# Kernel tuning notes

Hardware: AMD Instinct MI355X
Metric: run time of the kernel (lower is better)

## Reference

```python
import jax, jax.numpy as jnp
import numpy as np

GRID = 8
Q = GRID * GRID


def _resize(x, hw):
    # F.interpolate(mode='bilinear', align_corners=False) == jax.image.resize bilinear (half-pixel)
    return jax.image.resize(x, (x.shape[0], x.shape[1], hw[0], hw[1]), method='bilinear')


def _transform(l1, l2, l3):
    hw = l1.shape[2:]
    return jnp.concatenate([l1, _resize(l2, hw), _resize(l3, hw)], axis=1)


def _mlp(x, w1, b1, w2, b2):
    return jax.nn.relu(x @ w1 + b1) @ w2 + b2


def setup_inputs():
    key = jax.random.key(0)
    ks = jax.random.split(key, 16)
    B = 4
    inp = {}
    shapes = {
        't0_l0': (B, 64, 128, 128), 't0_l1': (B, 256, 128, 128),
        't0_l2': (B, 256, 64, 64), 't0_l3': (B, 256, 32, 32),
        't1_l0': (B, 64, 128, 128), 't1_l1': (B, 256, 128, 128),
        't1_l2': (B, 256, 64, 64), 't1_l3': (B, 256, 32, 32),
    }
    for i, (n, s) in enumerate(shapes.items()):
        inp[n] = jax.random.normal(ks[i], s, dtype=jnp.float32)
    # init_query_bbox: (grid + 0.5) / grid_size, exactly as _init_layers
    xx, yy = jnp.meshgrid(jnp.arange(GRID), jnp.arange(GRID), indexing='ij')
    inp['query_bbox'] = (jnp.stack([xx, yy], -1).reshape(Q, 2).astype(jnp.float32) + 0.5) / GRID
    D = 256
    inp['off_w1'] = jax.random.normal(ks[8], (D, D // 2), dtype=jnp.float32) * 0.05
    inp['off_b1'] = jnp.zeros((D // 2,), jnp.float32)
    inp['off_w2'] = jax.random.normal(ks[9], (D // 2, 2), dtype=jnp.float32) * 0.05
    inp['off_b2'] = jnp.zeros((2,), jnp.float32)
    inp['sc_w1'] = jax.random.normal(ks[10], (D, D // 2), dtype=jnp.float32) * 0.05
    inp['sc_b1'] = jnp.zeros((D // 2,), jnp.float32)
    inp['sc_w2'] = jax.random.normal(ks[11], (D // 2, 1), dtype=jnp.float32) * 0.05
    inp['sc_b2'] = jnp.zeros((1,), jnp.float32)
    return inp


def reference(t0_l0, t0_l1, t0_l2, t0_l3, t1_l0, t1_l1, t1_l2, t1_l3,
              query_bbox, off_w1, off_b1, off_w2, off_b2, sc_w1, sc_b1, sc_w2, sc_b2):
    features = _transform(t0_l1, t0_l2, t0_l3)        # [B, 3C, H, W]
    features_next = _transform(t1_l1, t1_l2, t1_l3)
    B, C, H, W = features.shape
    shape = W
    w = W // GRID // 2                                 # half patch width (=8)
    qb = jnp.broadcast_to(query_bbox[None], (B, Q, 2))
    cp = (qb * shape).astype(jnp.int32)                # [B,Q,2] integer centers

    # ---- make_query_feat: batched patch gather (source uses batch-0 centers for all samples)
    mean_feat = features.mean(axis=1)                  # [B,H,W]
    cp0 = cp[0]                                        # [Q,2]
    rows = cp0[:, 0, None] - w + jnp.arange(2 * w)     # [Q,2w]
    cols = cp0[:, 1, None] - w + jnp.arange(2 * w)     # [Q,2w]
    patches = mean_feat[:, rows[:, :, None], cols[:, None, :]]  # [B,Q,2w,2w]
    D = 4 * w * w
    # source does torch.cat(list_over_q, dim=0).reshape(B, Q, -1): this interleaves
    # query/batch axes; replicate faithfully via transpose-then-reshape
    query_feat = jnp.transpose(patches.reshape(B, Q, D), (1, 0, 2)).reshape(B, Q, D)

    offset = _mlp(query_feat, off_w1, off_b1, off_w2, off_b2)   # [B,Q,2]
    scale = _mlp(query_feat, sc_w1, sc_b1, sc_w2, sc_b2)        # [B,Q,1]
    qb_new = (cp.astype(offset.dtype) + offset * w) / shape

    cps = (qb_new * shape).astype(jnp.int32)           # trunc toward zero == torch .to(int32)
    rs, cs = cps[..., 0] - w, cps[..., 1] - w          # [B,Q]
    re_, ce_ = cps[..., 0] + w, cps[..., 1] + w
    r = jnp.arange(H)
    c = jnp.arange(W)
    # torch slicing: negative start wraps to an empty slice -> require start >= 0;
    # end beyond H/W is clipped automatically by r < re_
    row_m = (r[None, None, :] >= rs[..., None]) & (r[None, None, :] < re_[..., None]) & (rs[..., None] >= 0)
    col_m = (c[None, None, :] >= cs[..., None]) & (c[None, None, :] < ce_[..., None]) & (cs[..., None] >= 0)
    cov = row_m[:, :, :, None] & col_m[:, :, None, :]  # [B,Q,H,W]
    tag = jnp.where(cov, jnp.arange(1, Q + 1)[None, :, None, None], 0)
    last = tag.max(axis=1)                             # [B,H,W]; 0 => pixel untouched
    sw = scale[..., 0]                                 # [B,Q]
    sm = jnp.take_along_axis(sw, jnp.maximum(last - 1, 0).reshape(B, -1), axis=1).reshape(B, H, W)
    scale_map = jnp.where(last > 0, sm, jnp.ones((), sw.dtype))
    return features * scale_map[:, None] + features_next
```

## Files before the change

### kernel.cpp

```cpp
#include <hip/hip_runtime.h>

#define HW1 16384
#define HW2 4096
#define HW3 1024
#define NB  4
#define NCH 256

typedef float f4 __attribute__((ext_vector_type(4)));

__device__ inline float psum8(const float* __restrict__ P, int stride, int idx) {
    float s = 0.f;
    #pragma unroll
    for (int g = 0; g < 8; ++g) s += P[(size_t)g * stride + idx];
    return s;
}

__device__ inline float bilp(const float* __restrict__ P, int stride, int n,
                             int y, int x, float scl, float off) {
    float fy = y * scl - off, fx = x * scl - off;
    float fy0 = floorf(fy), fx0 = floorf(fx);
    float wy = fy - fy0, wx = fx - fx0;
    int y0 = max((int)fy0, 0), y1 = min((int)fy0 + 1, n - 1);
    int x0 = max((int)fx0, 0), x1 = min((int)fx0 + 1, n - 1);
    float m00 = psum8(P, stride, y0 * n + x0), m01 = psum8(P, stride, y0 * n + x1);
    float m10 = psum8(P, stride, y1 * n + x0), m11 = psum8(P, stride, y1 * n + x1);
    float a = m00 * (1.f - wx) + m01 * wx;
    float b = m10 * (1.f - wx) + m11 * wx;
    return a * (1.f - wy) + b * wy;
}

__global__ __launch_bounds__(256) void k_sumsA(
    const float* __restrict__ l1, const float* __restrict__ l2, const float* __restrict__ l3,
    float* __restrict__ P1, float* __restrict__ P2, float* __restrict__ P3) {
    int t = threadIdx.x, blk = blockIdx.x;
    const float* src; float* dst; int hw, px0, b, cg;
    if (blk < 512) {
        b = blk >> 7; cg = (blk >> 4) & 7; int q = blk & 15;
        hw = HW1; src = l1; dst = P1; px0 = q * 1024;
    } else if (blk < 640) {
        int k = blk - 512; b = k >> 5; cg = (k >> 2) & 7; int q = k & 3;
        hw = HW2; src = l2; dst = P2; px0 = q * 1024;
    } else {
        int k = blk - 640; b = k >> 3; cg = k & 7;
        hw = HW3; src = l3; dst = P3; px0 = 0;
    }
    const f4* s = (const f4*)(src + ((size_t)(b * NCH + cg * 32)) * hw + px0);
    int hw4 = hw >> 2;
    f4 acc = {0.f, 0.f, 0.f, 0.f};
    #pragma unroll 8
    for (int c = 0; c < 32; ++c)
        acc += s[(size_t)c * hw4 + t];
    ((f4*)(dst + ((size_t)(b * 8 + cg)) * hw + px0))[t] = acc;
}

__global__ __launch_bounds__(256) void k_query(
    const float* __restrict__ P1, const float* __restrict__ P2, const float* __restrict__ P3,
    const float* __restrict__ qb,
    const float* __restrict__ ow1, const float* __restrict__ ob1,
    const float* __restrict__ ow2, const float* __restrict__ ob2,
    const float* __restrict__ sw1, const float* __restrict__ sb1,
    const float* __restrict__ sw2, const float* __restrict__ sb2,
    int* __restrict__ RS, int* __restrict__ CS, float* __restrict__ SC) {
    __shared__ float feat[256];
    __shared__ float hid[256];
    __shared__ float res[3];
    int n = blockIdx.x, t = threadIdx.x;
    int b = n & 3, qp = n >> 2;
    int qi = qp >> 3, qj = qp & 7;
    {
        int i = t >> 4, j = t & 15;
        int y = 16 * qi + i, x = 16 * qj + j;
        const float* P1b = P1 + (size_t)b * 8 * HW1;
        const float* P2b = P2 + (size_t)b * 8 * HW2;
        const float* P3b = P3 + (size_t)b * 8 * HW3;
        float v = psum8(P1b, HW1, y * 128 + x);
        v += bilp(P2b, HW2, 64, y, x, 0.5f, 0.25f);
        v += bilp(P3b, HW3, 32, y, x, 0.25f, 0.375f);
        feat[t] = v * (1.0f / 768.0f);
    }
    __syncthreads();
    {
        int h = t & 127;
        const float* W  = (t < 128) ? ow1 : sw1;
        const float* Bv = (t < 128) ? ob1 : sb1;
        float acc = 0.f;
        #pragma unroll 8
        for (int d = 0; d < 256; ++d)
            acc = fmaf(feat[d], W[d * 128 + h], acc);
        hid[t] = fmaxf(acc + Bv[h], 0.f);
    }
    __syncthreads();
    int w = t >> 6, l = t & 63;
    if (w < 3) {
        float acc;
        if (w == 0)      acc = fmaf(hid[l], ow2[2 * l],     hid[l + 64] * ow2[2 * l + 128]);
        else if (w == 1) acc = fmaf(hid[l], ow2[2 * l + 1], hid[l + 64] * ow2[2 * l + 129]);
        else             acc = fmaf(hid[128 + l], sw2[l],   hid[192 + l] * sw2[l + 64]);
        #pragma unroll
        for (int off = 32; off; off >>= 1) acc += __shfl_down(acc, off);
        if (l == 0) res[w] = acc + (w == 0 ? ob2[0] : (w == 1 ? ob2[1] : sb2[0]));
    }
    __syncthreads();
    if (t == 0) {
        int q = n & 63;
        int cpx = (int)(qb[2 * q + 0] * 128.0f);
        int cpy = (int)(qb[2 * q + 1] * 128.0f);
        int cpsx = (int)((float)cpx + res[0] * 8.0f);
        int cpsy = (int)((float)cpy + res[1] * 8.0f);
        RS[n] = cpsx - 8;
        CS[n] = cpsy - 8;
        SC[n] = res[2];
    }
}

__global__ __launch_bounds__(256) void k_scalemap(
    const int* __restrict__ RS, const int* __restrict__ CS, const float* __restrict__ SC,
    float* __restrict__ SMAP) {
    __shared__ int rs[64], cs[64];
    __shared__ float sc[64];
    int t = threadIdx.x;
    int p = blockIdx.x * 256 + t;
    int b = p >> 14;
    if (t < 64) { rs[t] = RS[b * 64 + t]; cs[t] = CS[b * 64 + t]; sc[t] = SC[b * 64 + t]; }
    __syncthreads();
    int off = p & (HW1 - 1);
    int r = off >> 7, c = off & 127;
    float sv = 1.0f;
    for (int q = 63; q >= 0; --q) {
        int r0 = rs[q], c0 = cs[q];
        if (r0 >= 0 && c0 >= 0 && (unsigned)(r - r0) < 16u && (unsigned)(c - c0) < 16u) {
            sv = sc[q]; break;
        }
    }
    SMAP[p] = sv;
}

__global__ __launch_bounds__(256) void k_direct(
    const float* __restrict__ a1, const float* __restrict__ n1,
    const float* __restrict__ SMAP, float* __restrict__ out) {
    int t = threadIdx.x;
    int plane = blockIdx.x >> 1;
    int half  = blockIdx.x & 1;
    int b  = plane >> 8;
    int ch = plane & 255;
    const f4* f  = (const f4*)(a1 + ((size_t)(b * 256 + ch)) * HW1);
    const f4* fn = (const f4*)(n1 + ((size_t)(b * 256 + ch)) * HW1);
    const f4* s4 = (const f4*)(SMAP + b * HW1);
    f4* o4 = (f4*)(out + ((size_t)(b * 768 + ch)) * HW1);
    int base = half * 2048;
    #pragma unroll
    for (int k = 0; k < 8; ++k) {
        int i = base + k * 256 + t;
        f4 fv = f[i];
        f4 sv = s4[i];
        f4 nv = __builtin_nontemporal_load(&fn[i]);
        f4 r;
        r.x = fmaf(fv.x, sv.x, nv.x);
        r.y = fmaf(fv.y, sv.y, nv.y);
        r.z = fmaf(fv.z, sv.z, nv.z);
        r.w = fmaf(fv.w, sv.w, nv.w);
        o4[i] = r;
    }
}

__global__ __launch_bounds__(256, 4) void k_up(
    const float* __restrict__ a2, const float* __restrict__ a3,
    const float* __restrict__ n2, const float* __restrict__ n3,
    const float* __restrict__ SMAP, float* __restrict__ out) {
    __shared__ float cur[4096];
    __shared__ float nxt[4096];
    int t = threadIdx.x;
    int c_local = blockIdx.x >> 2;
    int b = blockIdx.x & 3;
    const f4* s4 = (const f4*)(SMAP + b * HW1);
    const size_t obase = (size_t)(b * 768) * HW1;

    {
        const f4* s0 = (const f4*)(a2 + ((size_t)(b * 256 + c_local)) * HW2);
        const f4* s1 = (const f4*)(n2 + ((size_t)(b * 256 + c_local)) * HW2);
        f4* o4 = (f4*)(out + obase + (size_t)(256 + c_local) * HW1);
        for (int i = t; i < 1024; i += 256) {
            ((f4*)cur)[i] = s0[i];
            ((f4*)nxt)[i] = __builtin_nontemporal_load(&s1[i]);
        }
        __syncthreads();
        for (int i = t; i < 4096; i += 256) {
            int y = i >> 5, j = i & 31;
            int iy = (y - 1) >> 1;
            int y0 = max(iy, 0), y1 = min(iy + 1, 63);
            float wy = (y & 1) ? 0.25f : 0.75f;
            int cm1 = max(2 * j - 1, 0);
            int c0 = 2 * j, c1 = 2 * j + 1;
            int c2c = min(2 * j + 2, 63);
            const float* r0 = cur + y0 * 64; const float* r1 = cur + y1 * 64;
            const float* u0 = nxt + y0 * 64; const float* u1 = nxt + y1 * 64;
            float a0 = r0[cm1], a1v = r0[c0], a2v = r0[c1], a3v = r0[c2c];
            float b0 = r1[cm1], b1v = r1[c0], b2v = r1[c1], b3v = r1[c2c];
            float p0 = u0[cm1], p1 = u0[c0], p2 = u0[c1], p3 = u0[c2c];
            float q0 = u1[cm1], q1 = u1[c0], q2 = u1[c1], q3 = u1[c2c];
            float h0 = fmaf(0.25f, a0, 0.75f * a1v);
            float h1 = fmaf(0.75f, a1v, 0.25f * a2v);
            float h2 = fmaf(0.25f, a1v, 0.75f * a2v);
            float h3 = fmaf(0.75f, a2v, 0.25f * a3v);
            float g0 = fmaf(0.25f, b0, 0.75f * b1v);
            float g1 = fmaf(0.75f, b1v, 0.25f * b2v);
            float g2 = fmaf(0.25f, b1v, 0.75f * b2v);
            float g3 = fmaf(0.75f, b2v, 0.25f * b3v);
            float e0 = fmaf(0.25f, p0, 0.75f * p1);
            float e1 = fmaf(0.75f, p1, 0.25f * p2);
            float e2 = fmaf(0.25f, p1, 0.75f * p2);
            float e3 = fmaf(0.75f, p2, 0.25f * p3);
            float k0 = fmaf(0.25f, q0, 0.75f * q1);
            float k1 = fmaf(0.75f, q1, 0.25f * q2);
            float k2 = fmaf(0.25f, q1, 0.75f * q2);
            float k3 = fmaf(0.75f, q2, 0.25f * q3);
            f4 sv = s4[i];
            f4 r;
            r.x = fmaf(fmaf(g0 - h0, wy, h0), sv.x, fmaf(k0 - e0, wy, e0));
            r.y = fmaf(fmaf(g1 - h1, wy, h1), sv.y, fmaf(k1 - e1, wy, e1));
            r.z = fmaf(fmaf(g2 - h2, wy, h2), sv.z, fmaf(k2 - e2, wy, e2));
            r.w = fmaf(fmaf(g3 - h3, wy, h3), sv.w, fmaf(k3 - e3, wy, e3));
            o4[i] = r;
        }
    }

    __syncthreads();

    {
        const f4* s0 = (const f4*)(a3 + ((size_t)(b * 256 + c_local)) * HW3);
        const f4* s1 = (const f4*)(n3 + ((size_t)(b * 256 + c_local)) * HW3);
        f4* o4 = (f4*)(out + obase + (size_t)(512 + c_local) * HW1);
        for (int i = t; i < 256; i += 256) {
            ((f4*)cur)[i] = s0[i];
            ((f4*)nxt)[i] = __builtin_nontemporal_load(&s1[i]);
        }
        __syncthreads();
        for (int i = t; i < 4096; i += 256) {
            int y = i >> 5, j = i & 31;
            int iy = (y - 2) >> 2;
            int y0 = max(iy, 0), y1 = min(iy + 1, 31);
            int ym = y & 3;
            float wy = (ym < 2) ? (0.625f + 0.25f * ym) : (0.25f * ym - 0.375f);
            int cm1 = max(j - 1, 0);
            int c0 = j, c1 = min(j + 1, 31);
            const float* r0 = cur + y0 * 32; const float* r1 = cur + y1 * 32;
            const float* u0 = nxt + y0 * 32; const float* u1 = nxt + y1 * 32;
            float a0 = r0[cm1], a1v = r0[c0], a2v = r0[c1];
            float b0 = r1[cm1], b1v = r1[c0], b2v = r1[c1];
            float p0 = u0[cm1], p1 = u0[c0], p2 = u0[c1];
            float q0 = u1[cm1], q1 = u1[c0], q2 = u1[c1];
            float h0 = fmaf(0.375f, a0, 0.625f * a1v);
            float h1 = fmaf(0.125f, a0, 0.875f * a1v);
            float h2 = fmaf(0.875f, a1v, 0.125f * a2v);
            float h3 = fmaf(0.625f, a1v, 0.375f * a2v);
            float g0 = fmaf(0.375f, b0, 0.625f * b1v);
            float g1 = fmaf(0.125f, b0, 0.875f * b1v);
            float g2 = fmaf(0.875f, b1v, 0.125f * b2v);
            float g3 = fmaf(0.625f, b1v, 0.375f * b2v);
            float e0 = fmaf(0.375f, p0, 0.625f * p1);
            float e1 = fmaf(0.125f, p0, 0.875f * p1);
            float e2 = fmaf(0.875f, p1, 0.125f * p2);
            float e3 = fmaf(0.625f, p1, 0.375f * p2);
            float k0 = fmaf(0.375f, q0, 0.625f * q1);
            float k1 = fmaf(0.125f, q0, 0.875f * q1);
            float k2 = fmaf(0.875f, q1, 0.125f * q2);
            float k3 = fmaf(0.625f, q1, 0.375f * q2);
            f4 sv = s4[i];
            f4 r;
            r.x = fmaf(fmaf(g0 - h0, wy, h0), sv.x, fmaf(k0 - e0, wy, e0));
            r.y = fmaf(fmaf(g1 - h1, wy, h1), sv.y, fmaf(k1 - e1, wy, e1));
            r.z = fmaf(fmaf(g2 - h2, wy, h2), sv.z, fmaf(k2 - e2, wy, e2));
            r.w = fmaf(fmaf(g3 - h3, wy, h3), sv.w, fmaf(k3 - e3, wy, e3));
            o4[i] = r;
        }
    }
}

extern "C" void kernel_launch(void* const* d_in, const int* in_sizes, int n_in,
                              void* d_out, int out_size, void* d_ws, size_t ws_size,
                              hipStream_t stream) {
    (void)in_sizes; (void)n_in; (void)out_size; (void)ws_size;
    const float* t0_l1 = (const float*)d_in[1];
    const float* t0_l2 = (const float*)d_in[2];
    const float* t0_l3 = (const float*)d_in[3];
    const float* t1_l1 = (const float*)d_in[5];
    const float* t1_l2 = (const float*)d_in[6];
    const float* t1_l3 = (const float*)d_in[7];
    const float* qb    = (const float*)d_in[8];
    const float* ow1   = (const float*)d_in[9];
    const float* ob1   = (const float*)d_in[10];
    const float* ow2   = (const float*)d_in[11];
    const float* ob2   = (const float*)d_in[12];
    const float* sw1   = (const float*)d_in[13];
    const float* sb1   = (const float*)d_in[14];
    const float* sw2   = (const float*)d_in[15];
    const float* sb2   = (const float*)d_in[16];

    char* ws = (char*)d_ws;
    float* P1   = (float*)(ws + 0);
    float* P2   = (float*)(ws + 2097152);
    float* P3   = (float*)(ws + 2621440);
    int*   RS   = (int*)  (ws + 2752512);
    int*   CS   = (int*)  (ws + 2753536);
    float* SC   = (float*)(ws + 2754560);
    float* SMAP = (float*)(ws + 2755584);
    float* out  = (float*)d_out;

    hipLaunchKernelGGL(k_sumsA, dim3(672), dim3(256), 0, stream,
                       t0_l1, t0_l2, t0_l3, P1, P2, P3);
    hipLaunchKernelGGL(k_query, dim3(256), dim3(256), 0, stream,
                       P1, P2, P3, qb, ow1, ob1, ow2, ob2, sw1, sb1, sw2, sb2, RS, CS, SC);
    hipLaunchKernelGGL(k_scalemap, dim3(256), dim3(256), 0, stream, RS, CS, SC, SMAP);
    hipLaunchKernelGGL(k_direct, dim3(2048), dim3(256), 0, stream,
                       t0_l1, t1_l1, SMAP, out);
    hipLaunchKernelGGL(k_up, dim3(1024), dim3(256), 0, stream,
                       t0_l2, t0_l3, t1_l2, t1_l3, SMAP, out);
}
```

Baseline: 105.2 us.

## Batch eight queries per block in query MLP and drop nontemporal loads

```diff
diff --git a/kernel.cpp b/kernel.cpp
--- a/kernel.cpp
+++ b/kernel.cpp
@@ -3,7 +3,6 @@
 #define HW1 16384
 #define HW2 4096
 #define HW3 1024
-#define NB  4
 #define NCH 256
 
 typedef float f4 __attribute__((ext_vector_type(4)));
@@ -61,55 +60,67 @@
     const float* __restrict__ sw1, const float* __restrict__ sb1,
     const float* __restrict__ sw2, const float* __restrict__ sb2,
     int* __restrict__ RS, int* __restrict__ CS, float* __restrict__ SC) {
-    __shared__ float feat[256];
-    __shared__ float hid[256];
-    __shared__ float res[3];
-    int n = blockIdx.x, t = threadIdx.x;
-    int b = n & 3, qp = n >> 2;
-    int qi = qp >> 3, qj = qp & 7;
-    {
-        int i = t >> 4, j = t & 15;
+    __shared__ float feat[8][256];
+    __shared__ float hid[2][8][128];
+    __shared__ float res[8][3];
+    int t = threadIdx.x;
+    int n0 = blockIdx.x * 8;
+
+    for (int v = t; v < 2048; v += 256) {
+        int r = v >> 8, d = v & 255;
+        int n = n0 + r;
+        int b = n & 3, qp = n >> 2;
+        int qi = qp >> 3, qj = qp & 7;
+        int i = d >> 4, j = d & 15;
         int y = 16 * qi + i, x = 16 * qj + j;
         const float* P1b = P1 + (size_t)b * 8 * HW1;
         const float* P2b = P2 + (size_t)b * 8 * HW2;
         const float* P3b = P3 + (size_t)b * 8 * HW3;
-        float v = psum8(P1b, HW1, y * 128 + x);
-        v += bilp(P2b, HW2, 64, y, x, 0.5f, 0.25f);
-        v += bilp(P3b, HW3, 32, y, x, 0.25f, 0.375f);
-        feat[t] = v * (1.0f / 768.0f);
-    }
-    __syncthreads();
+        float val = psum8(P1b, HW1, y * 128 + x);
+        val += bilp(P2b, HW2, 64, y, x, 0.5f, 0.25f);
+        val += bilp(P3b, HW3, 32, y, x, 0.25f, 0.375f);
+        feat[r][d] = val * (1.0f / 768.0f);
+    }
+    __syncthreads();
+
     {
-        int h = t & 127;
-        const float* W  = (t < 128) ? ow1 : sw1;
-        const float* Bv = (t < 128) ? ob1 : sb1;
+        int m = t >> 7, h = t & 127;
+        const float* W  = m ? sw1 : ow1;
+        float bias = (m ? sb1 : ob1)[h];
+        float acc[8];
+        #pragma unroll
+        for (int r = 0; r < 8; ++r) acc[r] = 0.f;
+        for (int d = 0; d < 256; ++d) {
+            float w = W[d * 128 + h];
+            #pragma unroll
+            for (int r = 0; r < 8; ++r)
+                acc[r] = fmaf(feat[r][d], w, acc[r]);
+        }
+        #pragma unroll
+        for (int r = 0; r < 8; ++r)
+            hid[m][r][h] = fmaxf(acc[r] + bias, 0.f);
+    }
+    __syncthreads();
+
+    if (t < 24) {
+        int r = t / 3, o = t - r * 3;
         float acc = 0.f;
-        #pragma unroll 8
-        for (int d = 0; d < 256; ++d)
-            acc = fmaf(feat[d], W[d * 128 + h], acc);
-        hid[t] = fmaxf(acc + Bv[h], 0.f);
-    }
-    __syncthreads();
-    int w = t >> 6, l = t & 63;
-    if (w < 3) {
-        float acc;
-        if (w == 0)      acc = fmaf(hid[l], ow2[2 * l],     hid[l + 64] * ow2[2 * l + 128]);
-        else if (w == 1) acc = fmaf(hid[l], ow2[2 * l + 1], hid[l + 64] * ow2[2 * l + 129]);
-        else             acc = fmaf(hid[128 + l], sw2[l],   hid[192 + l] * sw2[l + 64]);
-        #pragma unroll
-        for (int off = 32; off; off >>= 1) acc += __shfl_down(acc, off);
-        if (l == 0) res[w] = acc + (w == 0 ? ob2[0] : (w == 1 ? ob2[1] : sb2[0]));
-    }
-    __syncthreads();
-    if (t == 0) {
-        int q = n & 63;
+        if (o == 0)      { for (int j = 0; j < 128; ++j) acc = fmaf(hid[0][r][j], ow2[2 * j],     acc); acc += ob2[0]; }
+        else if (o == 1) { for (int j = 0; j < 128; ++j) acc = fmaf(hid[0][r][j], ow2[2 * j + 1], acc); acc += ob2[1]; }
+        else             { for (int j = 0; j < 128; ++j) acc = fmaf(hid[1][r][j], sw2[j],         acc); acc += sb2[0]; }
+        res[r][o] = acc;
+    }
+    __syncthreads();
+
+    if (t < 8) {
+        int n = n0 + t, q = n & 63;
         int cpx = (int)(qb[2 * q + 0] * 128.0f);
         int cpy = (int)(qb[2 * q + 1] * 128.0f);
-        int cpsx = (int)((float)cpx + res[0] * 8.0f);
-        int cpsy = (int)((float)cpy + res[1] * 8.0f);
+        int cpsx = (int)((float)cpx + res[t][0] * 8.0f);
+        int cpsy = (int)((float)cpy + res[t][1] * 8.0f);
         RS[n] = cpsx - 8;
         CS[n] = cpsy - 8;
-        SC[n] = res[2];
+        SC[n] = res[t][2];
     }
 }
 
@@ -153,7 +164,7 @@
         int i = base + k * 256 + t;
         f4 fv = f[i];
         f4 sv = s4[i];
-        f4 nv = __builtin_nontemporal_load(&fn[i]);
+        f4 nv = fn[i];
         f4 r;
         r.x = fmaf(fv.x, sv.x, nv.x);
         r.y = fmaf(fv.y, sv.y, nv.y);
@@ -181,7 +192,7 @@
         f4* o4 = (f4*)(out + obase + (size_t)(256 + c_local) * HW1);
         for (int i = t; i < 1024; i += 256) {
             ((f4*)cur)[i] = s0[i];
-            ((f4*)nxt)[i] = __builtin_nontemporal_load(&s1[i]);
+            ((f4*)nxt)[i] = s1[i];
         }
         __syncthreads();
         for (int i = t; i < 4096; i += 256) {
@@ -232,7 +243,7 @@
         f4* o4 = (f4*)(out + obase + (size_t)(512 + c_local) * HW1);
         for (int i = t; i < 256; i += 256) {
             ((f4*)cur)[i] = s0[i];
-            ((f4*)nxt)[i] = __builtin_nontemporal_load(&s1[i]);
+            ((f4*)nxt)[i] = s1[i];
         }
         __syncthreads();
         for (int i = t; i < 4096; i += 256) {
@@ -308,7 +319,7 @@
 
     hipLaunchKernelGGL(k_sumsA, dim3(672), dim3(256), 0, stream,
                        t0_l1, t0_l2, t0_l3, P1, P2, P3);
-    hipLaunchKernelGGL(k_query, dim3(256), dim3(256), 0, stream,
+    hipLaunchKernelGGL(k_query, dim3(32), dim3(256), 0, stream,
                        P1, P2, P3, qb, ow1, ob1, ow2, ob2, sw1, sb1, sw2, sb2, RS, CS, SC);
     hipLaunchKernelGGL(k_scalemap, dim3(256), dim3(256), 0, stream, RS, CS, SC, SMAP);
     hipLaunchKernelGGL(k_direct, dim3(2048), dim3(256), 0, stream,
```

Measured after the change: 142.1 us. 35.1% more time.
